# Kernel tuning notes

Measured on AMD Instinct MI355X. Metric: run time of the kernel, lower is better.

The kernel has to match this reference:

```python
import jax, jax.numpy as jnp
import numpy as np

NQ = 16   # n_qubits
NL = 3    # feature-map layers
M = 20    # molecule_size
B = 32


def setup_inputs() -> dict:
    key = jax.random.key(0)
    ks = jax.random.split(key, 12)
    s = 0.1
    return {
        "molecular_coordinates": jax.random.normal(ks[0], (B, M, 3), jnp.float32),
        "molecular_features": jax.random.normal(ks[1], (B, 100), jnp.float32),
        "rotation_params": jax.random.normal(ks[2], (NL, NQ, 3), jnp.float32),
        "entangling_params": jax.random.normal(ks[3], (NL, NQ - 1), jnp.float32),
        "fp_w1": jax.random.normal(ks[4], (64, 100), jnp.float32) * s,
        "fp_b1": jnp.zeros((64,), jnp.float32),
        "fp_w2": jax.random.normal(ks[5], (NQ, 64), jnp.float32) * s,
        "fp_b2": jnp.zeros((NQ,), jnp.float32),
        "hc_w1": jax.random.normal(ks[6], (256, M * 3), jnp.float32) * s,
        "hc_b1": jnp.zeros((256,), jnp.float32),
        "hc_w2": jax.random.normal(ks[7], (128, 256), jnp.float32) * s,
        "hc_b2": jnp.zeros((128,), jnp.float32),
        "hc_w3": jax.random.normal(ks[8], (NQ * NQ, 128), jnp.float32) * s,
        "hc_b3": jnp.zeros((NQ * NQ,), jnp.float32),
    }


def _apply_rotation(amps, q, R):
    # amps: (B, 2^NQ) complex; R: (B, 2, 2) complex. Single-qubit gate on qubit q
    # (bit q has stride 2^q): reshape to expose that bit and contract with R.
    b = amps.shape[0]
    a = amps.reshape(b, 2 ** (NQ - q - 1), 2, 2 ** q)
    return jnp.einsum('bij,bhjl->bhil', R, a).reshape(b, 2 ** NQ)


def _apply_cnot(amps, c, p):
    # Soft CNOT on control=c, target=c+1. Net effect of the torch loop: for
    # control bit == 1, new[s] = (1-p)*a[s] + p*a[s ^ (1<<target)].
    b = amps.shape[0]
    a = amps.reshape(b, 2 ** (NQ - c - 2), 2, 2, 2 ** c)  # [high, t_bit, c_bit, low]
    t0 = a[:, :, 0, 1, :]
    t1 = a[:, :, 1, 1, :]
    a = a.at[:, :, 0, 1, :].set((1 - p) * t0 + p * t1)
    a = a.at[:, :, 1, 1, :].set((1 - p) * t1 + p * t0)
    return a.reshape(b, 2 ** NQ)


def _feature_map(features, rot, ent, w1, b1, w2, b2):
    pf = jnp.tanh(jax.nn.relu(features @ w1.T + b1) @ w2.T + b2)  # (B, NQ)
    b = features.shape[0]
    amps = jnp.zeros((b, 2 ** NQ), jnp.complex64).at[:, 0].set(1.0)
    for layer in range(NL):
        for q in range(NQ):
            rx = rot[layer, q, 0] * pf[:, q]
            ry = rot[layer, q, 1] * pf[:, q]
            rz = rot[layer, q, 2] * pf[:, q]
            cx, sx = jnp.cos(rx / 2), jnp.sin(rx / 2)
            cy, sy = jnp.cos(ry / 2), jnp.sin(ry / 2)
            cz, sz = jnp.cos(rz / 2), jnp.sin(rz / 2)
            row0 = jnp.stack([cx * cy * cz, -sx * sy * sz], axis=-1)
            row1 = jnp.stack([sx * sy * cz, cx * cy * sz], axis=-1)
            R = jnp.stack([row0, row1], axis=1).astype(jnp.complex64)  # (B,2,2)
            amps = _apply_rotation(amps, q, R)
        for q in range(NQ - 1):
            p = jax.nn.sigmoid(ent[layer, q]).astype(jnp.complex64)
            amps = _apply_cnot(amps, q, p)
    return amps


def _hamiltonian(coords, w1, b1, w2, b2, w3, b3):
    b = coords.shape[0]
    x = coords.reshape(b, -1)  # (B, 60)
    h = jax.nn.relu(x @ w1.T + b1)
    h = jax.nn.relu(h @ w2.T + b2)
    h = (h @ w3.T + b3).reshape(b, NQ, NQ)
    h = (h + jnp.swapaxes(h, -1, -2)) / 2
    # torch.var is unbiased (ddof=1); same frequency added to every diagonal entry
    var = jnp.var(x, axis=1, ddof=1)
    freq = jnp.sqrt(1.0 / (var + 1e-6)) * 200.0
    return h + freq[:, None, None] * jnp.eye(NQ, dtype=h.dtype)


def _forward(molecular_coordinates, molecular_features, rotation_params,
             entangling_params, fp_w1, fp_b1, fp_w2, fp_b2,
             hc_w1, hc_b1, hc_w2, hc_b2, hc_w3, hc_b3):
    H = _hamiltonian(molecular_coordinates, hc_w1, hc_b1, hc_w2, hc_b2, hc_w3, hc_b3)
    amps = _feature_map(molecular_features, rotation_params, entangling_params,
                        fp_w1, fp_b1, fp_w2, fp_b2)
    b = amps.shape[0]
    # pack state (re/im) and Hamiltonian into one real output
    return jnp.concatenate([amps.real, amps.imag, H.reshape(b, -1)], axis=1)


def reference(molecular_coordinates, molecular_features, rotation_params,
              entangling_params, fp_w1, fp_b1, fp_w2, fp_b2,
              hc_w1, hc_b1, hc_w2, hc_b2, hc_w3, hc_b3):
    return _forward(molecular_coordinates, molecular_features, rotation_params,
                    entangling_params, fp_w1, fp_b1, fp_w2, fp_b2,
                    hc_w1, hc_b1, hc_w2, hc_b2, hc_w3, hc_b3)
```

## Files before the change

### kernel.cpp

```cpp
#include <hip/hip_runtime.h>
#include <math.h>

#define NSTATE 65536
#define OUTSTRIDE 131328


#define RP(A,B) { float t=A; A = t*g00 + B*g10; B = B*g11 + t*g01; }
#define RB0 RP(r0,r1) RP(r2,r3) RP(r4,r5) RP(r6,r7)
#define RB1 RP(r0,r2) RP(r1,r3) RP(r4,r6) RP(r5,r7)
#define RB2 RP(r0,r4) RP(r1,r5) RP(r2,r6) RP(r3,r7)
#define RRB(l,q,BITS) { const float* gg = sc + ((l)*16+(q))*4; \
  const float g00=gg[0], g01=gg[1], g10=gg[2], g11=gg[3]; BITS }
#define EP(A,B) { float t=A; A = (1.f-p)*A + p*B; B = (1.f-p)*B + p*t; }
#define REB0(l) { const float p = sc[192+(l)*15+0]; EP(r1,r3) EP(r5,r7) }
#define REB1(l) { const float p = sc[192+(l)*15+1]; EP(r2,r6) EP(r3,r7) }
#define ROWINIT r0=(om==0)?1.f:0.f; r1=(om==1)?1.f:0.f; r2=(om==2)?1.f:0.f; \
  r3=(om==3)?1.f:0.f; r4=(om==4)?1.f:0.f; r5=(om==5)?1.f:0.f; \
  r6=(om==6)?1.f:0.f; r7=(om==7)?1.f:0.f;

#define SH4(v) { float ox=__shfl_xor(v.x,msk,64), oy=__shfl_xor(v.y,msk,64), \
                       oz=__shfl_xor(v.z,msk,64), ow=__shfl_xor(v.w,msk,64); \
  v.x=cown*v.x+coth*ox; v.y=cown*v.y+coth*oy; v.z=cown*v.z+coth*oz; v.w=cown*v.w+coth*ow; }
#define ROTL(l,q) { const float* gg = sc + ((l)*16+(q))*4; \
  const float g00=gg[0], g01=gg[1], g10=gg[2], g11=gg[3]; \
  const int msk = 1<<((q)-3); const int lb = (lane>>((q)-3))&1; \
  const float cown = lb?g11:g00, coth = lb?g10:g01; SH4(v0) SH4(v1) }
#define ROTW(l,q) { const float* gg = sc + ((l)*16+(q))*4; \
  const float g00=gg[0], g01=gg[1], g10=gg[2], g11=gg[3]; \
  const int k=(q)-9; const int bt=(wv>>k)&1; \
  const float cown = bt?g11:g00, coth = bt?g10:g01; \
  const int pb = ((wv^(1<<k))<<6)|lane; \
  __syncthreads(); xbuf[tid]=v0; xbuf[1024+tid]=v1; __syncthreads(); \
  { float4 o=xbuf[pb];      v0.x=cown*v0.x+coth*o.x; v0.y=cown*v0.y+coth*o.y; \
                            v0.z=cown*v0.z+coth*o.z; v0.w=cown*v0.w+coth*o.w; } \
  { float4 o=xbuf[1024+pb]; v1.x=cown*v1.x+coth*o.x; v1.y=cown*v1.y+coth*o.y; \
                            v1.z=cown*v1.z+coth*o.z; v1.w=cown*v1.w+coth*o.w; } }
#define ROT13(l) { const float* gg = sc + ((l)*16+13)*4; \
  const float g00=gg[0], g01=gg[1], g10=gg[2], g11=gg[3]; float nx,ny,nz,nw; \
  nx=g00*v0.x+g01*v0.y; ny=g10*v0.x+g11*v0.y; nz=g00*v0.z+g01*v0.w; nw=g10*v0.z+g11*v0.w; \
  v0.x=nx; v0.y=ny; v0.z=nz; v0.w=nw; \
  nx=g00*v1.x+g01*v1.y; ny=g10*v1.x+g11*v1.y; nz=g00*v1.z+g01*v1.w; nw=g10*v1.z+g11*v1.w; \
  v1.x=nx; v1.y=ny; v1.z=nz; v1.w=nw; }
#define ROT14(l) { const float* gg = sc + ((l)*16+14)*4; \
  const float g00=gg[0], g01=gg[1], g10=gg[2], g11=gg[3]; float nx,ny,nz,nw; \
  nx=g00*v0.x+g01*v0.z; nz=g10*v0.x+g11*v0.z; ny=g00*v0.y+g01*v0.w; nw=g10*v0.y+g11*v0.w; \
  v0.x=nx; v0.y=ny; v0.z=nz; v0.w=nw; \
  nx=g00*v1.x+g01*v1.z; nz=g10*v1.x+g11*v1.z; ny=g00*v1.y+g01*v1.w; nw=g10*v1.y+g11*v1.w; \
  v1.x=nx; v1.y=ny; v1.z=nz; v1.w=nw; }
#define ROT15(l) { const float* gg = sc + ((l)*16+15)*4; \
  const float g00=gg[0], g01=gg[1], g10=gg[2], g11=gg[3]; float t; \
  t=v0.x; v0.x=g00*t+g01*v1.x; v1.x=g10*t+g11*v1.x; \
  t=v0.y; v0.y=g00*t+g01*v1.y; v1.y=g10*t+g11*v1.y; \
  t=v0.z; v0.z=g00*t+g01*v1.z; v1.z=g10*t+g11*v1.z; \
  t=v0.w; v0.w=g00*t+g01*v1.w; v1.w=g10*t+g11*v1.w; }

#define ESH(v) { float ox=__shfl_xor(v.x,msk,64), oy=__shfl_xor(v.y,msk,64), \
                       oz=__shfl_xor(v.z,msk,64), ow=__shfl_xor(v.w,msk,64); \
  v.x+=pe*(ox-v.x); v.y+=pe*(oy-v.y); v.z+=pe*(oz-v.z); v.w+=pe*(ow-v.w); }
#define ENT2(l) { const float p = sc[192+(l)*15+2]; const float pe = (om&4)?p:0.f; \
  const int msk = 1; ESH(v0) ESH(v1) }
#define ENTL(l,c) { const float p = sc[192+(l)*15+(c)]; \
  const float pe = ((lane>>((c)-3))&1)?p:0.f; const int msk = 1<<((c)-2); ESH(v0) ESH(v1) }
#define ENT8(l) { const float p = sc[192+(l)*15+8]; \
  const float pe = ((lane>>5)&1)?p:0.f; const int pb = ((wv^1)<<6)|lane; \
  __syncthreads(); xbuf[tid]=v0; xbuf[1024+tid]=v1; __syncthreads(); \
  { float4 o=xbuf[pb];      v0.x+=pe*(o.x-v0.x); v0.y+=pe*(o.y-v0.y); \
                            v0.z+=pe*(o.z-v0.z); v0.w+=pe*(o.w-v0.w); } \
  { float4 o=xbuf[1024+pb]; v1.x+=pe*(o.x-v1.x); v1.y+=pe*(o.y-v1.y); \
                            v1.z+=pe*(o.z-v1.z); v1.w+=pe*(o.w-v1.w); } }
#define ENTW(l,c) { const float p = sc[192+(l)*15+(c)]; const int k=(c)-9; \
  const int cbv = (wv>>k)&1; const int pb = ((wv^(1<<(k+1)))<<6)|lane; \
  __syncthreads(); if(cbv){ xbuf[tid]=v0; xbuf[1024+tid]=v1; } __syncthreads(); \
  if(cbv){ float4 o=xbuf[pb];       v0.x+=p*(o.x-v0.x); v0.y+=p*(o.y-v0.y); \
                                    v0.z+=p*(o.z-v0.z); v0.w+=p*(o.w-v0.w); \
           float4 o1=xbuf[1024+pb]; v1.x+=p*(o1.x-v1.x); v1.y+=p*(o1.y-v1.y); \
                                    v1.z+=p*(o1.z-v1.z); v1.w+=p*(o1.w-v1.w); } }
#define ENT12(l) { const float p = sc[192+(l)*15+12]; const float pe = ((wv>>3)&1)?p:0.f; float d; \
  d=pe*(v0.y-v0.x); v0.x+=d; v0.y-=d;  d=pe*(v0.w-v0.z); v0.z+=d; v0.w-=d; \
  d=pe*(v1.y-v1.x); v1.x+=d; v1.y-=d;  d=pe*(v1.w-v1.z); v1.z+=d; v1.w-=d; }
#define ENT13(l) { const float p = sc[192+(l)*15+13]; float d; \
  d=p*(v0.w-v0.y); v0.y+=d; v0.w-=d;   d=p*(v1.w-v1.y); v1.y+=d; v1.w-=d; }
#define ENT14(l) { const float p = sc[192+(l)*15+14]; float d; \
  d=p*(v1.z-v0.z); v0.z+=d; v1.z-=d;   d=p*(v1.w-v0.w); v0.w+=d; v1.w-=d; }

#define ROTLOC(l) ROTL(l,3) ROTL(l,4) ROTL(l,5) ROTL(l,6) ROTL(l,7) ROTL(l,8) \
  ROTW(l,9) ROTW(l,10) ROTW(l,11) ROTW(l,12) ROT13(l) ROT14(l) ROT15(l)
#define ENTLOC(l) ENT2(l) ENTL(l,3) ENTL(l,4) ENTL(l,5) ENTL(l,6) ENTL(l,7) ENT8(l) \
  ENTW(l,9) ENTW(l,10) ENTW(l,11) ENT12(l) ENT13(l) ENT14(l)

#define GATH(SRC, J, ASSIGN) { \
  const float4* gp = (const float4*)((SRC) + ((J)<<13) + gb); \
  float4 lo = gp[0], hi = gp[1]; \
  float amp = r0*lo.x + r1*lo.y + r2*lo.z + r3*lo.w \
            + r4*hi.x + r5*hi.y + r6*hi.z + r7*hi.w; ASSIGN; }
#define GATHER8(SRC) \
  GATH(SRC,0, v0.x=amp) GATH(SRC,1, v0.y=amp) GATH(SRC,2, v0.z=amp) GATH(SRC,3, v0.w=amp) \
  GATH(SRC,4, v1.x=amp) GATH(SRC,5, v1.y=amp) GATH(SRC,6, v1.z=amp) GATH(SRC,7, v1.w=amp)

#define STORE8(DST) { float* dp = (DST); const int sb = (wv<<9)|(lane<<3)|om; \
  dp[sb + (0<<13)] = v0.x;  dp[sb + (1<<13)] = v0.y; \
  dp[sb + (2<<13)] = v0.z;  dp[sb + (3<<13)] = v0.w; \
  dp[sb + (4<<13)] = v1.x;  dp[sb + (5<<13)] = v1.y; \
  dp[sb + (6<<13)] = v1.z;  dp[sb + (7<<13)] = v1.w; }

typedef unsigned long long u64;
#define ASTORE64(P, V) __hip_atomic_store((P), (V), __ATOMIC_RELAXED, __HIP_MEMORY_SCOPE_AGENT)
#define ALOAD64(P)     __hip_atomic_load((P), __ATOMIC_RELAXED, __HIP_MEMORY_SCOPE_AGENT)

__device__ __forceinline__ u64 pk2(float a, float b) {
  union { float2 f; u64 u; } c; c.f = make_float2(a, b); return c.u;
}
__device__ __forceinline__ float2 upk2(u64 u) {
  union { u64 u; float2 f; } c; c.u = u; return c.f;
}

#define STORE8_WS(DST) { \
  u64* dp = (u64*)(DST) + ((om<<12)|(wv<<8)|lane); \
  ASTORE64(dp +   0, pk2(v0.x, v0.y));  ASTORE64(dp +  64, pk2(v0.z, v0.w)); \
  ASTORE64(dp + 128, pk2(v1.x, v1.y));  ASTORE64(dp + 192, pk2(v1.z, v1.w)); }

#define GW(SP, S, RS) { \
  float2 p0 = upk2(ALOAD64((SP) + ((S)<<12) +   0)); \
  float2 p1 = upk2(ALOAD64((SP) + ((S)<<12) +  64)); \
  float2 p2 = upk2(ALOAD64((SP) + ((S)<<12) + 128)); \
  float2 p3 = upk2(ALOAD64((SP) + ((S)<<12) + 192)); \
  v0.x += (RS)*p0.x; v0.y += (RS)*p0.y;  v0.z += (RS)*p1.x; v0.w += (RS)*p1.y; \
  v1.x += (RS)*p2.x; v1.y += (RS)*p2.y;  v1.z += (RS)*p3.x; v1.w += (RS)*p3.y; }

#define GATHER8_WS(SRC) { \
  const u64* sp = (const u64*)(SRC) + ((wv<<8)|lane); \
  v0 = make_float4(0.f,0.f,0.f,0.f);  v1 = make_float4(0.f,0.f,0.f,0.f); \
  GW(sp,0,r0) GW(sp,1,r1) GW(sp,2,r2) GW(sp,3,r3) \
  GW(sp,4,r4) GW(sp,5,r5) GW(sp,6,r6) GW(sp,7,r7) }

#define XSYNC(FP) { \
  asm volatile("s_waitcnt vmcnt(0)" ::: "memory"); \
  __syncthreads(); \
  if (tid == 0) { \
    __hip_atomic_fetch_add((FP), 1, __ATOMIC_RELAXED, __HIP_MEMORY_SCOPE_AGENT); \
    int guard = 0; \
    while (__hip_atomic_load((FP), __ATOMIC_RELAXED, __HIP_MEMORY_SCOPE_AGENT) < 8 \
           && ++guard < (1<<20)) __builtin_amdgcn_s_sleep(2); \
  } \
  __syncthreads(); }

__device__ __forceinline__ void compute_coefs(float* sc, int b, int tid,
    const float* feats, const float* rotp, const float* entp,
    const float* fpw1, const float* fpb1, const float* fpw2, const float* fpb2) {
  __shared__ float fh[64], pf[16];
  if (tid < 64) {
    float acc = fpb1[tid];
    const float* w = fpw1 + tid*100;
    const float* f = feats + b*100;
    for (int k = 0; k < 100; ++k) acc += w[k]*f[k];
    fh[tid] = fmaxf(acc, 0.f);
  } else if (tid < 64+45) {
    sc[192 + (tid-64)] = 1.f/(1.f + expf(-entp[tid-64]));
  }
  __syncthreads();
  if (tid < 16) {
    float acc = fpb2[tid];
    const float* w = fpw2 + tid*64;
    for (int k = 0; k < 64; ++k) acc += w[k]*fh[k];
    pf[tid] = tanhf(acc);
  }
  __syncthreads();
  if (tid < 48) {
    float ang = pf[tid & 15];
    const float* rp = rotp + tid*3;
    float cx = cosf(0.5f*rp[0]*ang), sx = sinf(0.5f*rp[0]*ang);
    float cy = cosf(0.5f*rp[1]*ang), sy = sinf(0.5f*rp[1]*ang);
    float cz = cosf(0.5f*rp[2]*ang), sz = sinf(0.5f*rp[2]*ang);
    float* cc = sc + tid*4;
    cc[0] =  cx*cy*cz; cc[1] = -sx*sy*sz; cc[2] = sx*sy*cz; cc[3] = cx*cy*sz;
  }
  __syncthreads();
}

__global__ __launch_bounds__(1024) void kF(
    const float* __restrict__ coords, const float* __restrict__ feats,
    const float* __restrict__ rotp,   const float* __restrict__ entp,
    const float* __restrict__ fpw1,   const float* __restrict__ fpb1,
    const float* __restrict__ fpw2,   const float* __restrict__ fpb2,
    const float* __restrict__ hcw1,   const float* __restrict__ hcb1,
    const float* __restrict__ hcw2,   const float* __restrict__ hcb2,
    const float* __restrict__ hcw3,   const float* __restrict__ hcb3,
    float* __restrict__ out, int* __restrict__ flags,
    float* __restrict__ w0, float* __restrict__ w1)
{
  const int tid = threadIdx.x, bid = blockIdx.x;

  if (bid >= 256) {
    __shared__ float xh[64], h1[256], h2[128], h3[256], ph[1024];
    const int b = bid - 256;
    if (tid < 60) xh[tid] = coords[b*60 + tid];
    __syncthreads();
    if (tid < 256) {
      float acc = hcb1[tid];
      const float* w = hcw1 + tid*60;
      for (int k = 0; k < 60; ++k) acc += w[k]*xh[k];
      h1[tid] = fmaxf(acc, 0.f);
    }
    __syncthreads();
    if (tid < 512) {
      int o = tid>>2, part = tid&3;
      float s = 0.f;
      const float* w = hcw2 + o*256 + part*64;
      const float* hh = h1 + part*64;
      for (int k = 0; k < 64; ++k) s += w[k]*hh[k];
      ph[tid] = s;
    }
    __syncthreads();
    if (tid < 128)
      h2[tid] = fmaxf(hcb2[tid] + ph[tid*4]+ph[tid*4+1]+ph[tid*4+2]+ph[tid*4+3], 0.f);
    __syncthreads();
    { int o = tid>>2, part = tid&3;
      float s = 0.f;
      const float* w = hcw3 + o*128 + part*32;
      const float* hh = h2 + part*32;
      for (int k = 0; k < 32; ++k) s += w[k]*hh[k];
      ph[tid] = s;
    }
    __syncthreads();
    if (tid < 256)
      h3[tid] = hcb3[tid] + ph[tid*4]+ph[tid*4+1]+ph[tid*4+2]+ph[tid*4+3];
    __syncthreads();
    if (tid < 256) {
      float s = 0.f, sq = 0.f;
      for (int k = 0; k < 60; ++k) { float v = xh[k]; s += v; sq += v*v; }
      float mean = s*(1.f/60.f);
      float var  = (sq - 60.f*mean*mean)*(1.f/59.f);
      float freq = sqrtf(1.f/(var + 1e-6f))*200.f;
      int i = tid >> 4, j = tid & 15;
      out[(size_t)b*OUTSTRIDE + 2*NSTATE + tid] =
          0.5f*(h3[tid] + h3[j*16 + i]) + ((i==j) ? freq : 0.f);
    }
    return;
  }

  __shared__ float4 xbuf[2048];
  __shared__ float sc[240];
  const int b = bid & 31, om = bid >> 5;
  const int lane = tid & 63, wv = tid >> 6;

  compute_coefs(sc, b, tid, feats, rotp, entp, fpw1, fpb1, fpw2, fpb2);

  float4 v0, v1;
  float r0, r1, r2, r3, r4, r5, r6, r7;

  ROWINIT
  RRB(1,1,RB1) RRB(1,0,RB0) REB1(0) REB0(0) RRB(0,2,RB2) RRB(0,1,RB1) RRB(0,0,RB0)
  {
    const float d = r0;
    float L = 1.f;
    for (int q = 3; q <= 8; ++q) {
      const float* gg = sc + q*4;
      L *= ((lane >> (q-3)) & 1) ? gg[2] : gg[0];
    }
    float W = 1.f;
    for (int q = 9; q <= 12; ++q) {
      const float* gg = sc + q*4;
      W *= ((wv >> (q-9)) & 1) ? gg[2] : gg[0];
    }
    const float base = d * L * W;
    const float a13 = sc[13*4], b13 = sc[13*4+2];
    const float a14 = sc[14*4], b14 = sc[14*4+2];
    const float a15 = sc[15*4], b15 = sc[15*4+2];
    v0.x = base*a13*a14*a15;  v0.y = base*b13*a14*a15;
    v0.z = base*a13*b14*a15;  v0.w = base*b13*b14*a15;
    v1.x = base*a13*a14*b15;  v1.y = base*b13*a14*b15;
    v1.z = base*a13*b14*b15;  v1.w = base*b13*b14*b15;
  }
  ENTLOC(0) ROTLOC(1)
  STORE8_WS(w0 + (size_t)b*65536)
  {
    float4* oz = (float4*)(out + (size_t)b*OUTSTRIDE + NSTATE + om*8192);
    const float4 z = make_float4(0.f, 0.f, 0.f, 0.f);
    oz[tid] = z;
    oz[1024 + tid] = z;
  }

  XSYNC(flags + b)

  ROWINIT
  RRB(2,1,RB1) RRB(2,0,RB0) REB1(1) REB0(1) RRB(1,2,RB2)
  GATHER8_WS(w0 + (size_t)b*65536)
  ENTLOC(1) ROTLOC(2)
  STORE8_WS(w1 + (size_t)b*65536)

  XSYNC(flags + 32 + b)

  ROWINIT
  REB1(2) REB0(2) RRB(2,2,RB2)
  GATHER8_WS(w1 + (size_t)b*65536)
  ENTLOC(2)
  STORE8(out + (size_t)b*OUTSTRIDE)
}


template<bool ZIMAG>
__global__ __launch_bounds__(1024) void kA(
    const float* __restrict__ coords, const float* __restrict__ feats,
    const float* __restrict__ rotp,   const float* __restrict__ entp,
    const float* __restrict__ fpw1,   const float* __restrict__ fpb1,
    const float* __restrict__ fpw2,   const float* __restrict__ fpb2,
    const float* __restrict__ hcw1,   const float* __restrict__ hcb1,
    const float* __restrict__ hcw2,   const float* __restrict__ hcb2,
    const float* __restrict__ hcw3,   const float* __restrict__ hcb3,
    float* __restrict__ out, float* __restrict__ cws,
    float* __restrict__ dst, int dstride)
{
  __shared__ float4 xbuf[2048];
  __shared__ float sc[240];
  __shared__ float xh[64], h1[256], h2[128], h3[256], ph[1024];
  const int tid = threadIdx.x, bid = blockIdx.x;
  const int b = bid & 31, om = bid >> 5;
  const int lane = tid & 63, wv = tid >> 6;

  compute_coefs(sc, b, tid, feats, rotp, entp, fpw1, fpb1, fpw2, fpb2);
  if (cws != nullptr && om == 0 && tid < 240) cws[b*256 + tid] = sc[tid];

  if (om == 0) {
    if (tid < 60) xh[tid] = coords[b*60 + tid];
    __syncthreads();
    if (tid < 256) {
      float acc = hcb1[tid];
      const float* w = hcw1 + tid*60;
      for (int k = 0; k < 60; ++k) acc += w[k]*xh[k];
      h1[tid] = fmaxf(acc, 0.f);
    }
    __syncthreads();
    if (tid < 512) {
      int o = tid>>2, part = tid&3;
      float s = 0.f;
      const float* w = hcw2 + o*256 + part*64;
      const float* hh = h1 + part*64;
      for (int k = 0; k < 64; ++k) s += w[k]*hh[k];
      ph[tid] = s;
    }
    __syncthreads();
    if (tid < 128)
      h2[tid] = fmaxf(hcb2[tid] + ph[tid*4]+ph[tid*4+1]+ph[tid*4+2]+ph[tid*4+3], 0.f);
    __syncthreads();
    { int o = tid>>2, part = tid&3;
      float s = 0.f;
      const float* w = hcw3 + o*128 + part*32;
      const float* hh = h2 + part*32;
      for (int k = 0; k < 32; ++k) s += w[k]*hh[k];
      ph[tid] = s;
    }
    __syncthreads();
    if (tid < 256)
      h3[tid] = hcb3[tid] + ph[tid*4]+ph[tid*4+1]+ph[tid*4+2]+ph[tid*4+3];
    __syncthreads();
    if (tid < 256) {
      float s = 0.f, sq = 0.f;
      for (int k = 0; k < 60; ++k) { float v = xh[k]; s += v; sq += v*v; }
      float mean = s*(1.f/60.f);
      float var  = (sq - 60.f*mean*mean)*(1.f/59.f);
      float freq = sqrtf(1.f/(var + 1e-6f))*200.f;
      int i = tid >> 4, j = tid & 15;
      out[(size_t)b*OUTSTRIDE + 2*NSTATE + tid] =
          0.5f*(h3[tid] + h3[j*16 + i]) + ((i==j) ? freq : 0.f);
    }
  }

  float4 v0, v1;
  float r0, r1, r2, r3, r4, r5, r6, r7;
  ROWINIT
  RRB(1,1,RB1) RRB(1,0,RB0) REB1(0) REB0(0) RRB(0,2,RB2) RRB(0,1,RB1) RRB(0,0,RB0)
  const float d = r0;
  float L = 1.f;
  for (int q = 3; q <= 8; ++q) {
    const float* gg = sc + q*4;
    L *= ((lane >> (q-3)) & 1) ? gg[2] : gg[0];
  }
  float W = 1.f;
  for (int q = 9; q <= 12; ++q) {
    const float* gg = sc + q*4;
    W *= ((wv >> (q-9)) & 1) ? gg[2] : gg[0];
  }
  const float base = d * L * W;
  const float a13 = sc[13*4], b13 = sc[13*4+2];
  const float a14 = sc[14*4], b14 = sc[14*4+2];
  const float a15 = sc[15*4], b15 = sc[15*4+2];
  v0.x = base*a13*a14*a15;  v0.y = base*b13*a14*a15;
  v0.z = base*a13*b14*a15;  v0.w = base*b13*b14*a15;
  v1.x = base*a13*a14*b15;  v1.y = base*b13*a14*b15;
  v1.z = base*a13*b14*b15;  v1.w = base*b13*b14*b15;
  ENTLOC(0) ROTLOC(1)
  STORE8(dst + (size_t)b*dstride)

  if constexpr (ZIMAG) {
    float4* oz = (float4*)(out + (size_t)b*OUTSTRIDE + NSTATE + om*8192);
    const float4 z = make_float4(0.f, 0.f, 0.f, 0.f);
    oz[tid] = z;
    oz[1024 + tid] = z;
  }
}

template<bool LOADC>
__global__ __launch_bounds__(1024) void kB(
    const float* __restrict__ feats, const float* __restrict__ rotp,
    const float* __restrict__ entp,  const float* __restrict__ fpw1,
    const float* __restrict__ fpb1,  const float* __restrict__ fpw2,
    const float* __restrict__ fpb2,  const float* __restrict__ cws,
    const float* __restrict__ src, int sstride,
    float* __restrict__ dst, int dstride)
{
  __shared__ float4 xbuf[2048];
  __shared__ float sc[240];
  const int tid = threadIdx.x, bid = blockIdx.x;
  const int b = bid & 31, om = bid >> 5;
  const int lane = tid & 63, wv = tid >> 6;
  if constexpr (LOADC) {
    for (int i = tid; i < 240; i += 1024) sc[i] = cws[b*256 + i];
    __syncthreads();
  } else {
    compute_coefs(sc, b, tid, feats, rotp, entp, fpw1, fpb1, fpw2, fpb2);
  }
  float4 v0, v1;
  float r0, r1, r2, r3, r4, r5, r6, r7;
  const int gb = (wv<<9) | (lane<<3);
  ROWINIT
  RRB(2,1,RB1) RRB(2,0,RB0) REB1(1) REB0(1) RRB(1,2,RB2)
  GATHER8(src + (size_t)b*sstride)
  ENTLOC(1) ROTLOC(2)
  STORE8(dst + (size_t)b*dstride)
}

template<bool LOADC>
__global__ __launch_bounds__(1024) void kC(
    const float* __restrict__ feats, const float* __restrict__ rotp,
    const float* __restrict__ entp,  const float* __restrict__ fpw1,
    const float* __restrict__ fpb1,  const float* __restrict__ fpw2,
    const float* __restrict__ fpb2,  const float* __restrict__ cws,
    const float* __restrict__ src, int sstride,
    float* __restrict__ dst, int dstride)
{
  __shared__ float4 xbuf[2048];
  __shared__ float sc[240];
  const int tid = threadIdx.x, bid = blockIdx.x;
  const int b = bid & 31, om = bid >> 5;
  const int lane = tid & 63, wv = tid >> 6;
  if constexpr (LOADC) {
    for (int i = tid; i < 240; i += 1024) sc[i] = cws[b*256 + i];
    __syncthreads();
  } else {
    compute_coefs(sc, b, tid, feats, rotp, entp, fpw1, fpb1, fpw2, fpb2);
  }
  float4 v0, v1;
  float r0, r1, r2, r3, r4, r5, r6, r7;
  const int gb = (wv<<9) | (lane<<3);
  ROWINIT
  REB1(2) REB0(2) RRB(2,2,RB2)
  GATHER8(src + (size_t)b*sstride)
  ENTLOC(2)
  STORE8(dst + (size_t)b*dstride)
}

__global__ __launch_bounds__(1024) void kD(float* __restrict__ out) {
  const int tid = threadIdx.x, bid = blockIdx.x;
  const int b = bid & 31, om = bid >> 5;
  float4* rr = (float4*)(out + (size_t)b*OUTSTRIDE + om*8192);
  float4* im = (float4*)(out + (size_t)b*OUTSTRIDE + NSTATE + om*8192);
  const float4 z = make_float4(0.f, 0.f, 0.f, 0.f);
  float4 a = im[tid], c = im[1024 + tid];
  rr[tid] = a;  rr[1024 + tid] = c;
  im[tid] = z;  im[1024 + tid] = z;
}

extern "C" void kernel_launch(void* const* d_in, const int* in_sizes, int n_in,
                              void* d_out, int out_size, void* d_ws, size_t ws_size,
                              hipStream_t stream) {
  const float* coords = (const float*)d_in[0];
  const float* feats  = (const float*)d_in[1];
  const float* rotp   = (const float*)d_in[2];
  const float* entp   = (const float*)d_in[3];
  const float* fpw1   = (const float*)d_in[4];
  const float* fpb1   = (const float*)d_in[5];
  const float* fpw2   = (const float*)d_in[6];
  const float* fpb2   = (const float*)d_in[7];
  const float* hcw1   = (const float*)d_in[8];
  const float* hcb1   = (const float*)d_in[9];
  const float* hcw2   = (const float*)d_in[10];
  const float* hcb2   = (const float*)d_in[11];
  const float* hcw3   = (const float*)d_in[12];
  const float* hcb3   = (const float*)d_in[13];
  float* out = (float*)d_out;
  float* wsf = (float*)d_ws;
  const size_t need_fused = (size_t)(1024 + 2*32*65536) * 4;

  if (ws_size >= need_fused) {
    int*   flags = (int*)wsf;
    float* w0 = wsf + 1024;
    float* w1 = w0 + 32*65536;
    hipMemsetAsync(wsf, 0, 256, stream);
    kF<<<288, 1024, 0, stream>>>(coords, feats, rotp, entp,
        fpw1, fpb1, fpw2, fpb2, hcw1, hcb1, hcw2, hcb2, hcw3, hcb3,
        out, flags, w0, w1);
  } else if (ws_size >= 32768) {
    float* cws = wsf;
    kA<false><<<256, 1024, 0, stream>>>(coords, feats, rotp, entp,
        fpw1, fpb1, fpw2, fpb2, hcw1, hcb1, hcw2, hcb2, hcw3, hcb3,
        out, cws, out + NSTATE, OUTSTRIDE);
    kB<true><<<256, 1024, 0, stream>>>(feats, rotp, entp, fpw1, fpb1, fpw2, fpb2,
        cws, out + NSTATE, OUTSTRIDE, out, OUTSTRIDE);
    kC<true><<<256, 1024, 0, stream>>>(feats, rotp, entp, fpw1, fpb1, fpw2, fpb2,
        cws, out, OUTSTRIDE, out + NSTATE, OUTSTRIDE);
    kD<<<256, 1024, 0, stream>>>(out);
  } else {
    kA<false><<<256, 1024, 0, stream>>>(coords, feats, rotp, entp,
        fpw1, fpb1, fpw2, fpb2, hcw1, hcb1, hcw2, hcb2, hcw3, hcb3,
        out, nullptr, out + NSTATE, OUTSTRIDE);
    kB<false><<<256, 1024, 0, stream>>>(feats, rotp, entp, fpw1, fpb1, fpw2, fpb2,
        nullptr, out + NSTATE, OUTSTRIDE, out, OUTSTRIDE);
    kC<false><<<256, 1024, 0, stream>>>(feats, rotp, entp, fpw1, fpb1, fpw2, fpb2,
        nullptr, out, OUTSTRIDE, out + NSTATE, OUTSTRIDE);
    kD<<<256, 1024, 0, stream>>>(out);
  }
}
```

Measured before the change: 140.1 us.

## Replace block-wide barriers in cross-wave gate exchanges with pairwise LDS flag sync

The cross-wave rotation and entangling steps for qubits 8-12 now use per-wave write/read flags in shared memory instead of __syncthreads. A wave waits only on its partner wave, and the LDS exchange buffer is doubled so consecutive gates alternate halves. This is meant to cut the cost of full-workgroup barriers and let waves run ahead independently. The price is spin-wait polling, a larger LDS footprint that may lower occupancy, and a subtle memory-ordering risk from relaxed atomics combined with manual waitcnt.

```diff
diff --git a/kernel.cpp b/kernel.cpp
--- a/kernel.cpp
+++ b/kernel.cpp
@@ -88,6 +88,66 @@
 #define ENTLOC(l) ENT2(l) ENTL(l,3) ENTL(l,4) ENTL(l,5) ENTL(l,6) ENTL(l,7) ENT8(l) \
   ENTW(l,9) ENTW(l,10) ENTW(l,11) ENT12(l) ENT13(l) ENT14(l)
 
+#define SIGW(G) { asm volatile("s_waitcnt lgkmcnt(0)" ::: "memory"); \
+  if (lane == 0) __hip_atomic_store(&wrf[wv], (G), __ATOMIC_RELAXED, __HIP_MEMORY_SCOPE_WORKGROUP); }
+#define SIGR(G) { asm volatile("s_waitcnt lgkmcnt(0)" ::: "memory"); \
+  if (lane == 0) __hip_atomic_store(&rdf[wv], (G), __ATOMIC_RELAXED, __HIP_MEMORY_SCOPE_WORKGROUP); }
+#define WAITF(ARR, W, V) { int _gd = 0; \
+  while (__hip_atomic_load(&(ARR)[W], __ATOMIC_RELAXED, __HIP_MEMORY_SCOPE_WORKGROUP) < (V) \
+         && ++_gd < (1<<22)) {} }
+#define WARW(G) { if ((G) >= 3) WAITF(rdf, wv^(1<<(((G)-3)&3)), (G)-2) }
+
+#define ROTWG(l,q,G) { const float* gg = sc + ((l)*16+(q))*4; \
+  const float g00=gg[0], g01=gg[1], g10=gg[2], g11=gg[3]; \
+  const int k=(q)-9; const int bt=(wv>>k)&1; \
+  const float cown = bt?g11:g00, coth = bt?g10:g01; \
+  const int pb = ((wv^(1<<k))<<6)|lane; \
+  float4* xb = xbuf + (((G)&1)<<11); \
+  WARW(G) \
+  xb[tid]=v0; xb[1024+tid]=v1; \
+  SIGW(G) \
+  WAITF(wrf, wv^(1<<k), G) \
+  { float4 o=xb[pb];      v0.x=cown*v0.x+coth*o.x; v0.y=cown*v0.y+coth*o.y; \
+                          v0.z=cown*v0.z+coth*o.z; v0.w=cown*v0.w+coth*o.w; } \
+  { float4 o=xb[1024+pb]; v1.x=cown*v1.x+coth*o.x; v1.y=cown*v1.y+coth*o.y; \
+                          v1.z=cown*v1.z+coth*o.z; v1.w=cown*v1.w+coth*o.w; } \
+  SIGR(G) }
+
+#define ENT8G(l,G) { const float p = sc[192+(l)*15+8]; \
+  const float pe = ((lane>>5)&1)?p:0.f; const int pb = ((wv^1)<<6)|lane; \
+  float4* xb = xbuf + (((G)&1)<<11); \
+  WARW(G) \
+  xb[tid]=v0; xb[1024+tid]=v1; \
+  SIGW(G) \
+  WAITF(wrf, wv^1, G) \
+  { float4 o=xb[pb];      v0.x+=pe*(o.x-v0.x); v0.y+=pe*(o.y-v0.y); \
+                          v0.z+=pe*(o.z-v0.z); v0.w+=pe*(o.w-v0.w); } \
+  { float4 o=xb[1024+pb]; v1.x+=pe*(o.x-v1.x); v1.y+=pe*(o.y-v1.y); \
+                          v1.z+=pe*(o.z-v1.z); v1.w+=pe*(o.w-v1.w); } \
+  SIGR(G) }
+
+#define ENTWG(l,c,G) { const float p = sc[192+(l)*15+(c)]; const int k=(c)-9; \
+  const int cbv = (wv>>k)&1; const int pb = ((wv^(1<<(k+1)))<<6)|lane; \
+  float4* xb = xbuf + (((G)&1)<<11); \
+  if (cbv) { \
+    WARW(G) \
+    xb[tid]=v0; xb[1024+tid]=v1; \
+    SIGW(G) \
+    WAITF(wrf, wv^(1<<(k+1)), G) \
+    { float4 o=xb[pb];       v0.x+=p*(o.x-v0.x); v0.y+=p*(o.y-v0.y); \
+                             v0.z+=p*(o.z-v0.z); v0.w+=p*(o.w-v0.w); } \
+    { float4 o1=xb[1024+pb]; v1.x+=p*(o1.x-v1.x); v1.y+=p*(o1.y-v1.y); \
+                             v1.z+=p*(o1.z-v1.z); v1.w+=p*(o1.w-v1.w); } \
+    SIGR(G) \
+  } else { SIGW(G) SIGR(G) } }
+
+#define ENTLOCG(l,B) ENT2(l) ENTL(l,3) ENTL(l,4) ENTL(l,5) ENTL(l,6) ENTL(l,7) \
+  ENT8G(l,(B)+1) ENTWG(l,9,(B)+2) ENTWG(l,10,(B)+3) ENTWG(l,11,(B)+4) \
+  ENT12(l) ENT13(l) ENT14(l)
+#define ROTLOCG(l,B) ROTL(l,3) ROTL(l,4) ROTL(l,5) ROTL(l,6) ROTL(l,7) ROTL(l,8) \
+  ROTWG(l,9,(B)+5) ROTWG(l,10,(B)+6) ROTWG(l,11,(B)+7) ROTWG(l,12,(B)+8) \
+  ROT13(l) ROT14(l) ROT15(l)
+
 #define GATH(SRC, J, ASSIGN) { \
   const float4* gp = (const float4*)((SRC) + ((J)<<13) + gb); \
   float4 lo = gp[0], hi = gp[1]; \
@@ -238,11 +298,13 @@
     return;
   }
 
-  __shared__ float4 xbuf[2048];
+  __shared__ float4 xbuf[4096];
+  __shared__ int wrf[16], rdf[16];
   __shared__ float sc[240];
   const int b = bid & 31, om = bid >> 5;
   const int lane = tid & 63, wv = tid >> 6;
 
+  if (tid < 16) { wrf[tid] = 0; rdf[tid] = 0; }
   compute_coefs(sc, b, tid, feats, rotp, entp, fpw1, fpb1, fpw2, fpb2);
 
   float4 v0, v1;
@@ -271,7 +333,7 @@
     v1.x = base*a13*a14*b15;  v1.y = base*b13*a14*b15;
     v1.z = base*a13*b14*b15;  v1.w = base*b13*b14*b15;
   }
-  ENTLOC(0) ROTLOC(1)
+  ENTLOCG(0,0) ROTLOCG(1,0)
   STORE8_WS(w0 + (size_t)b*65536)
   {
     float4* oz = (float4*)(out + (size_t)b*OUTSTRIDE + NSTATE + om*8192);
@@ -285,7 +347,7 @@
   ROWINIT
   RRB(2,1,RB1) RRB(2,0,RB0) REB1(1) REB0(1) RRB(1,2,RB2)
   GATHER8_WS(w0 + (size_t)b*65536)
-  ENTLOC(1) ROTLOC(2)
+  ENTLOCG(1,8) ROTLOCG(2,8)
   STORE8_WS(w1 + (size_t)b*65536)
 
   XSYNC(flags + 32 + b)
@@ -293,7 +355,7 @@
   ROWINIT
   REB1(2) REB0(2) RRB(2,2,RB2)
   GATHER8_WS(w1 + (size_t)b*65536)
-  ENTLOC(2)
+  ENTLOCG(2,16)
   STORE8(out + (size_t)b*OUTSTRIDE)
 }
 
```

Result: slower. 144.1 us (+2.9%).
